# Kernel tuning notes

Measured on AMD Instinct MI355X. Metric: run time of the kernel, lower is better.

Reference implementation:

```python
import jax, jax.numpy as jnp
import numpy as np

Q = 16          # ELM-AE hidden size (init kwarg)
SPATIAL = 14    # spatial size of x[round(len(x)/2)] = x[2]
WH = SPATIAL * SPATIAL


def _zscore_nan(X):
    # torch_zscore(x, axis=0): normalize each pixel column over the z channels,
    # torch.std is unbiased (ddof=1); then torch.nan_to_num.
    mu = jnp.mean(X, axis=0)
    sd = jnp.std(X, axis=0, ddof=1)
    return jnp.nan_to_num((X - mu) / sd)


def _elm_member(xm, W):
    # xm: [b, z, wh] resized+flattened activation map; W: [Q, z] random encoder.
    def per_sample(Xs):                 # Xs: [z, wh]
        Xn = _zscore_nan(Xs)            # [z, wh]
        H = jax.nn.sigmoid(W @ Xn)      # [Q, wh] hidden representation
        B = Xn @ jnp.linalg.pinv(H)     # [z, Q]  closed-form AE decoder weights
        return jnp.var(B, axis=1, ddof=1)  # [z] variance pooling (Q > 1 branch)
    return jax.vmap(per_sample)(xm)     # [b, z]


def _forward(x0, x1, x2, x3, W0, W1, W2, W3):
    feats = []
    for xm, W in zip((x0, x1, x2, x3), (W0, W1, W2, W3)):
        b, c = xm.shape[0], xm.shape[1]
        xr = jax.image.resize(xm, (b, c, SPATIAL, SPATIAL), method='bilinear')
        feats.append(_elm_member(xr.reshape(b, c, WH), W))
    return jnp.concatenate(feats, axis=1)  # [b, sum_z] == torch.stack(out)


def setup_inputs() -> dict:
    key = jax.random.key(0)
    ks = jax.random.split(key, 8)
    shapes = [(32, 256, 56, 56), (32, 512, 28, 28), (32, 1024, 14, 14), (32, 2048, 7, 7)]
    inp = {}
    for i, s in enumerate(shapes):
        inp[f'x{i}'] = jax.random.normal(ks[i], s, dtype=jnp.float32)
        # original: zscored LCG pseudo-random weights, shape [Q, z]
        inp[f'W{i}'] = jax.random.normal(ks[4 + i], (Q, s[1]), dtype=jnp.float32)
    return inp


def reference(x0, x1, x2, x3, W0, W1, W2, W3):
    return _forward(x0, x1, x2, x3, W0, W1, W2, W3)
```

## Files before the change

kernel.cpp:

```cpp
#include <hip/hip_runtime.h>
#include <math.h>

#define NB 32
#define NQ 16
#define NP 196
#define OUTW 3840
#define HM_STRIDE (NQ * NP + NQ)
#define HM3_STRIDE (NQ * 49 + NQ)

template<int N>
__device__ __forceinline__ int calc_w(int i, float* w, int& lo) {
  constexpr float inv = (float)N / 14.0f;
  constexpr float ks  = (inv > 1.0f) ? inv : 1.0f;
  constexpr float rks = 1.0f / ks;
  float sf = ((float)i + 0.5f) * inv - 0.5f;
  int l = (int)ceilf(sf - ks);
  int h = (int)floorf(sf + ks);
  if (l < 0) l = 0;
  if (h > N - 1) h = N - 1;
  int n = h - l + 1;
  float sum = 0.f;
  for (int k = 0; k < n; ++k) {
    float t = 1.0f - fabsf((float)(l + k) - sf) * rks;
    t = t > 0.f ? t : 0.f;
    w[k] = t; sum += t;
  }
  float r = 1.0f / sum;
  for (int k = 0; k < n; ++k) w[k] *= r;
  for (int k = n; k < 8; ++k) w[k] = 0.f;
  lo = l;
  return n;
}

template<int N, int CH_BLK>
__global__ __launch_bounds__(256) void k_rs_mem(const float* __restrict__ x,
    const float* __restrict__ W, float* __restrict__ xr,
    float* __restrict__ part, int cm) {
  constexpr int TAPS = (N == 56) ? 8 : 4;
  constexpr int NROW = CH_BLK * N;
  constexpr int RV = N / 4;
  __shared__ float tmp[CH_BLK * N * 15];
  __shared__ float wxa[14 * 8], wya[14 * 8];
  __shared__ int lya[14], nya[14];
  __shared__ float wl[NQ * CH_BLK];
  const int t = threadIdx.x;
  const int s = blockIdx.x >> 5, chunk = blockIdx.x & 31;
  const int c0 = chunk * CH_BLK;

  if (t < 14)                 { int dum; calc_w<N>(t, &wxa[t * 8], dum); }
  else if (t >= 64 && t < 78) { int i = t - 64; nya[i] = calc_w<N>(i, &wya[i * 8], lya[i]); }
  for (int i = t; i < NQ * CH_BLK; i += 256) {
    int q = i / CH_BLK, cc = i - q * CH_BLK;
    wl[i] = W[q * cm + c0 + cc];
  }
  __syncthreads();

  for (int i = t; i < NROW; i += 256) {
    const int pl = i / N, r = i - pl * N;
    const float4* rp = (const float4*)(x + ((size_t)(s * cm + c0 + pl) * N + r) * N);
    float row[N];
#pragma unroll
    for (int j = 0; j < RV; ++j) {
      float4 f = rp[j];
      row[4 * j + 0] = f.x; row[4 * j + 1] = f.y;
      row[4 * j + 2] = f.z; row[4 * j + 3] = f.w;
    }
    float* td = &tmp[i * 15];
#pragma unroll
    for (int ox = 0; ox < 14; ++ox) {
      const int lx0 = (N == 56) ? (4 * ox - 2) : (2 * ox - 1);
      const int lx = lx0 < 0 ? 0 : lx0;
      float acc = 0.f;
#pragma unroll
      for (int k = 0; k < TAPS; ++k) {
        if (lx + k < N) acc = fmaf(wxa[ox * 8 + k], row[lx + k], acc);
      }
      td[ox] = acc;
    }
  }
  __syncthreads();

  if (t < NP) {
    const int oy = t / 14, ox = t - oy * 14;
    const int ny = nya[oy], ly = lya[oy];
    const float* wy = &wya[oy * 8];
    float s1 = 0.f, s2 = 0.f, y[NQ];
#pragma unroll
    for (int q = 0; q < NQ; ++q) y[q] = 0.f;
#pragma unroll
    for (int pl = 0; pl < CH_BLK; ++pl) {
      const float* tc = &tmp[(pl * N + ly) * 15 + ox];
      float acc = 0.f;
      for (int k = 0; k < ny; ++k) acc = fmaf(wy[k], tc[k * 15], acc);
      xr[((size_t)s * cm + c0 + pl) * NP + t] = acc;
      s1 += acc; s2 = fmaf(acc, acc, s2);
#pragma unroll
      for (int q = 0; q < NQ; ++q) y[q] = fmaf(wl[q * CH_BLK + pl], acc, y[q]);
    }
    float* pb = part + (size_t)(s * 32 + chunk) * 18 * NP + t;
    pb[0] = s1;
    pb[NP] = s2;
#pragma unroll
    for (int q = 0; q < NQ; ++q) pb[(size_t)(2 + q) * NP] = y[q];
  }
}

__global__ __launch_bounds__(256) void k_rs2(const float* __restrict__ x,
    const float* __restrict__ W, float* __restrict__ part) {
  const int t = threadIdx.x;
  if (t >= NP) return;
  const int s = blockIdx.x >> 5, chunk = blockIdx.x & 31;
  const int c0 = chunk * 32;
  const float* src = x + ((size_t)s * 1024 + c0) * NP + t;
  float s1 = 0.f, s2 = 0.f, y[NQ];
#pragma unroll
  for (int q = 0; q < NQ; ++q) y[q] = 0.f;
  for (int c = 0; c < 32; ++c) {
    float v = src[(size_t)c * NP];
    s1 += v; s2 = fmaf(v, v, s2);
#pragma unroll
    for (int q = 0; q < NQ; ++q) y[q] = fmaf(W[q * 1024 + c0 + c], v, y[q]);
  }
  float* pb = part + (size_t)(s * 32 + chunk) * 18 * NP + t;
  pb[0] = s1;
  pb[NP] = s2;
#pragma unroll
  for (int q = 0; q < NQ; ++q) pb[(size_t)(2 + q) * NP] = y[q];
}

__global__ __launch_bounds__(256) void k_rs3(const float* __restrict__ x,
    const float* __restrict__ W, float* __restrict__ part) {
  __shared__ __align__(16) float xl[64 * 49 + 16];
  __shared__ float wl[NQ * 64];
  __shared__ float w7a[14 * 8];
  __shared__ int l7a[14], n7a[14];
  const int t = threadIdx.x;
  const int s = blockIdx.x >> 5, chunk = blockIdx.x & 31;
  const int c0 = chunk * 64;

  if (t < 14) n7a[t] = calc_w<7>(t, &w7a[t * 8], l7a[t]);
  for (int i = t; i < NQ * 64; i += 256) {
    int q = i >> 6, cc = i & 63;
    wl[i] = W[q * 2048 + c0 + cc];
  }
  const float4* src4 = (const float4*)(x + ((size_t)s * 2048 + c0) * 49);
  float4* x4 = (float4*)xl;
  for (int i = t; i < 64 * 49 / 4; i += 256) x4[i] = src4[i];
  __syncthreads();

  if (t < NP) {
    const int oy = t / 14, ox = t - oy * 14;
    const int ly = l7a[oy], lx = l7a[ox];
    const float wy0 = w7a[oy * 8], wy1 = (n7a[oy] > 1) ? w7a[oy * 8 + 1] : 0.f;
    const float wx0 = w7a[ox * 8], wx1 = (n7a[ox] > 1) ? w7a[ox * 8 + 1] : 0.f;
    const int base0 = ly * 7 + lx;
    float s1 = 0.f, s2 = 0.f, y[NQ];
#pragma unroll
    for (int q = 0; q < NQ; ++q) y[q] = 0.f;
    for (int c = 0; c < 64; ++c) {
      const float* bb = &xl[c * 49 + base0];
      float v = wy0 * fmaf(wx1, bb[1], wx0 * bb[0]) + wy1 * fmaf(wx1, bb[8], wx0 * bb[7]);
      s1 += v; s2 = fmaf(v, v, s2);
#pragma unroll
      for (int q = 0; q < NQ; ++q) y[q] = fmaf(wl[q * 64 + c], v, y[q]);
    }
    float* pb = part + (size_t)(s * 32 + chunk) * 18 * NP + t;
    pb[0] = s1;
    pb[NP] = s2;
#pragma unroll
    for (int q = 0; q < NQ; ++q) pb[(size_t)(2 + q) * NP] = y[q];
  }
}

struct HeadArgs {
  const float* part[4];
  const float* W[4];
  float* hm[4];
  int cm[4];
};

__global__ __launch_bounds__(256) void k_head(HeadArgs A) {
  const int m = blockIdx.y, s = blockIdx.x, t = threadIdx.x;
  const int cm = A.cm[m];
  const float* W = A.W[m];
  const float* part = A.part[m];
  float* hm = A.hm[m];

  __shared__ float red[256];
  __shared__ float wsum[NQ];
  __shared__ float Hl[NQ * NP];
  __shared__ float HMl[NQ * NP];
  __shared__ float mul[NP], rsdl[NP];
  __shared__ float aug[16 * 33];
  __shared__ float Ml[256];
  __shared__ float el[NQ];
  __shared__ float w7[14 * 8];
  __shared__ int l7[14], n7[14];
  __shared__ float Radj[14 * 7];
  __shared__ float t2[NQ * 7 * 14];

  { int q = t >> 4, l = t & 15;
    float p = 0.f;
    for (int c = l; c < cm; c += 16) p += W[q * cm + c];
    red[t] = p; }
  __syncthreads();
  if (t < NQ) { float v = 0.f; for (int k = 0; k < 16; ++k) v += red[t * 16 + k]; wsum[t] = v; }
  __syncthreads();

  if (t < NP) {
    float s1 = 0.f, s2 = 0.f, y[NQ];
#pragma unroll
    for (int q = 0; q < NQ; ++q) y[q] = 0.f;
    for (int ch = 0; ch < 32; ++ch) {
      const float* pb = part + (size_t)(s * 32 + ch) * 18 * NP + t;
      s1 += pb[0];
      s2 += pb[NP];
#pragma unroll
      for (int q = 0; q < NQ; ++q) y[q] += pb[(size_t)(2 + q) * NP];
    }
    float mu = s1 / (float)cm;
    float var = (s2 - s1 * mu) / (float)(cm - 1);
    float rsd = (var > 0.f) ? (1.0f / sqrtf(var)) : 0.f;
    mul[t] = mu; rsdl[t] = rsd;
#pragma unroll
    for (int q = 0; q < NQ; ++q) {
      float arg = (y[q] - wsum[q] * mu) * rsd;
      Hl[q * NP + t] = 1.0f / (1.0f + expf(-arg));
    }
  }
  __syncthreads();

  { int q1 = t >> 4, q2 = t & 15;
    float g = 0.f;
    for (int p = 0; p < NP; ++p) g = fmaf(Hl[q1 * NP + p], Hl[q2 * NP + p], g);
    aug[q1 * 33 + q2] = g;
    aug[q1 * 33 + 16 + q2] = (q1 == q2) ? 1.0f : 0.f; }
  __syncthreads();

  for (int k = 0; k < 16; ++k) {
    float rpv = 1.0f / aug[k * 33 + k];
    __syncthreads();
    if (t < 32) aug[k * 33 + t] *= rpv;
    __syncthreads();
    int i = t >> 4, j = t & 15;
    float f = aug[i * 33 + k];
    __syncthreads();
    if (i != k) {
      aug[i * 33 + j]      -= f * aug[k * 33 + j];
      aug[i * 33 + 16 + j] -= f * aug[k * 33 + 16 + j];
    }
    __syncthreads();
  }
  { int i = t >> 4, j = t & 15; Ml[t] = aug[i * 33 + 16 + j]; }
  __syncthreads();

  if (t < NP) {
    float r_ = rsdl[t];
#pragma unroll
    for (int j = 0; j < NQ; ++j) {
      float acc = 0.f;
#pragma unroll
      for (int q = 0; q < NQ; ++q) acc = fmaf(Ml[j * 16 + q], Hl[q * NP + t], acc);
      HMl[j * NP + t] = acc * r_;
    }
  }
  __syncthreads();

  { int j = t >> 4, l = t & 15;
    float p = 0.f;
    for (int pp = l; pp < NP; pp += 16) p = fmaf(mul[pp], HMl[j * NP + pp], p);
    red[t] = p; }
  __syncthreads();
  if (t < NQ) { float v = 0.f; for (int k = 0; k < 16; ++k) v += red[t * 16 + k]; el[t] = v; }
  __syncthreads();

  if (m < 3) {
    float* dst = hm + (size_t)s * HM_STRIDE;
    for (int i = t; i < NQ * NP; i += 256) dst[i] = HMl[i];
    if (t < NQ) dst[NQ * NP + t] = el[t];
  } else {
    if (t < 14) n7[t] = calc_w<7>(t, &w7[t * 8], l7[t]);
    __syncthreads();
    if (t < 98) {
      int oy = t / 7, iy = t - oy * 7;
      int k = iy - l7[oy];
      Radj[oy * 7 + iy] = (k >= 0 && k < n7[oy]) ? w7[oy * 8 + k] : 0.f;
    }
    __syncthreads();
    for (int i = t; i < NQ * 7 * 14; i += 256) {
      int j = i / 98, rem = i - j * 98, iy = rem / 14, ox = rem - iy * 14;
      float acc = 0.f;
#pragma unroll
      for (int oy = 0; oy < 14; ++oy) acc = fmaf(Radj[oy * 7 + iy], HMl[j * NP + oy * 14 + ox], acc);
      t2[i] = acc;
    }
    __syncthreads();
    float* dst = hm + (size_t)s * HM3_STRIDE;
    for (int i = t; i < NQ * 49; i += 256) {
      int j = i / 49, rem = i - j * 49, iy = rem / 7, ix = rem - iy * 7;
      float acc = 0.f;
#pragma unroll
      for (int ox = 0; ox < 14; ++ox) acc = fmaf(Radj[ox * 7 + ix], t2[j * 98 + iy * 14 + ox], acc);
      dst[i] = acc;
    }
    if (t < NQ) dst[NQ * 49 + t] = el[t];
  }
}

#define CC3 32
struct VarArgs {
  const float* src[4];
  const float* hm[4];
  int cm[4];
  int ooff[4];
};

__global__ __launch_bounds__(512) void k_var(VarArgs A, float* __restrict__ out) {
  __shared__ __align__(16) float tile[CC3 * NP];
  __shared__ __align__(16) float hml[NQ * NP];
  __shared__ float el[NQ];
  int b = blockIdx.x;
  int m;
  if (b < 256)       { m = 0; }
  else if (b < 768)  { m = 1; b -= 256; }
  else if (b < 1792) { m = 2; b -= 768; }
  else               { m = 3; b -= 1792; }
  const int t = threadIdx.x;
  const int cc = t >> 4, j = t & 15;

  if (m < 3) {
    const int cm = A.cm[m];
    const int nch = cm / CC3;
    const int s = b / nch;
    const int ch = b % nch;
    const float4* src = (const float4*)(A.src[m] + ((size_t)s * cm + ch * CC3) * NP);
    float4* t4 = (float4*)tile;
    for (int i = t; i < CC3 * NP / 4; i += 512) t4[i] = src[i];
    const float4* hsrc = (const float4*)(A.hm[m] + (size_t)s * HM_STRIDE);
    float4* h4 = (float4*)hml;
    for (int i = t; i < NQ * NP / 4; i += 512) h4[i] = hsrc[i];
    if (t < NQ) el[t] = A.hm[m][(size_t)s * HM_STRIDE + NQ * NP + t];
    __syncthreads();

    const float4* tr = (const float4*)(tile + cc * NP);
    const float4* hr = (const float4*)(hml + j * NP);
    float acc = 0.f;
#pragma unroll 7
    for (int p4 = 0; p4 < NP / 4; ++p4) {
      float4 a = tr[p4], b2 = hr[p4];
      acc = fmaf(a.x, b2.x, acc);
      acc = fmaf(a.y, b2.y, acc);
      acc = fmaf(a.z, b2.z, acc);
      acc = fmaf(a.w, b2.w, acc);
    }
    float bv = acc - el[j];
    float s1 = bv;
    s1 += __shfl_xor(s1, 1, 16); s1 += __shfl_xor(s1, 2, 16);
    s1 += __shfl_xor(s1, 4, 16); s1 += __shfl_xor(s1, 8, 16);
    float mean = s1 * (1.0f / 16.0f);
    float d = bv - mean;
    float s2 = d * d;
    s2 += __shfl_xor(s2, 1, 16); s2 += __shfl_xor(s2, 2, 16);
    s2 += __shfl_xor(s2, 4, 16); s2 += __shfl_xor(s2, 8, 16);
    if (j == 0) out[(size_t)s * OUTW + A.ooff[m] + ch * CC3 + cc] = s2 * (1.0f / 15.0f);
  } else {
    const int s = b / 64;
    const int ch = b % 64;
    const float4* src = (const float4*)(A.src[3] + ((size_t)s * 2048 + ch * CC3) * 49);
    float4* t4 = (float4*)tile;
    for (int i = t; i < CC3 * 49 / 4; i += 512) t4[i] = src[i];
    const float4* hsrc = (const float4*)(A.hm[3] + (size_t)s * HM3_STRIDE);
    float4* h4 = (float4*)hml;
    for (int i = t; i < NQ * 49 / 4; i += 512) h4[i] = hsrc[i];
    if (t < NQ) el[t] = A.hm[3][(size_t)s * HM3_STRIDE + NQ * 49 + t];
    __syncthreads();

    const float* tr = tile + cc * 49;
    const float* hr = hml + j * 49;
    float acc = 0.f;
#pragma unroll
    for (int i = 0; i < 49; ++i) acc = fmaf(tr[i], hr[i], acc);
    float bv = acc - el[j];
    float s1 = bv;
    s1 += __shfl_xor(s1, 1, 16); s1 += __shfl_xor(s1, 2, 16);
    s1 += __shfl_xor(s1, 4, 16); s1 += __shfl_xor(s1, 8, 16);
    float mean = s1 * (1.0f / 16.0f);
    float d = bv - mean;
    float s2 = d * d;
    s2 += __shfl_xor(s2, 1, 16); s2 += __shfl_xor(s2, 2, 16);
    s2 += __shfl_xor(s2, 4, 16); s2 += __shfl_xor(s2, 8, 16);
    if (j == 0) out[(size_t)s * OUTW + 1792 + ch * CC3 + cc] = s2 * (1.0f / 15.0f);
  }
}

extern "C" void kernel_launch(void* const* d_in, const int* in_sizes, int n_in,
                              void* d_out, int out_size, void* d_ws, size_t ws_size,
                              hipStream_t stream) {
  const float* x0 = (const float*)d_in[0];
  const float* W0 = (const float*)d_in[1];
  const float* x1 = (const float*)d_in[2];
  const float* W1 = (const float*)d_in[3];
  const float* x2 = (const float*)d_in[4];
  const float* W2 = (const float*)d_in[5];
  const float* x3 = (const float*)d_in[6];
  const float* W3 = (const float*)d_in[7];
  float* out = (float*)d_out;
  float* ws = (float*)d_ws;

  float* xr0 = ws;
  float* xr1 = xr0 + (size_t)NB * 256 * NP;
  float* part0 = xr1 + (size_t)NB * 512 * NP;
  size_t plm = (size_t)NB * 32 * 18 * NP;
  float* part1 = part0 + plm;
  float* part2 = part1 + plm;
  float* part3 = part2 + plm;
  float* hm0 = part3 + plm;
  float* hm1 = hm0 + (size_t)NB * HM_STRIDE;
  float* hm2 = hm1 + (size_t)NB * HM_STRIDE;
  float* hm3 = hm2 + (size_t)NB * HM_STRIDE;

  k_rs_mem<56, 8><<<1024, 256, 0, stream>>>(x0, W0, xr0, part0, 256);
  k_rs_mem<28, 16><<<1024, 256, 0, stream>>>(x1, W1, xr1, part1, 512);
  k_rs2<<<1024, 256, 0, stream>>>(x2, W2, part2);
  k_rs3<<<1024, 256, 0, stream>>>(x3, W3, part3);

  HeadArgs A;
  A.part[0] = part0; A.part[1] = part1; A.part[2] = part2; A.part[3] = part3;
  A.W[0] = W0; A.W[1] = W1; A.W[2] = W2; A.W[3] = W3;
  A.hm[0] = hm0; A.hm[1] = hm1; A.hm[2] = hm2; A.hm[3] = hm3;
  A.cm[0] = 256; A.cm[1] = 512; A.cm[2] = 1024; A.cm[3] = 2048;
  k_head<<<dim3(NB, 4), 256, 0, stream>>>(A);

  VarArgs V;
  V.src[0] = xr0; V.src[1] = xr1; V.src[2] = x2; V.src[3] = x3;
  V.hm[0] = hm0; V.hm[1] = hm1; V.hm[2] = hm2; V.hm[3] = hm3;
  V.cm[0] = 256; V.cm[1] = 512; V.cm[2] = 1024; V.cm[3] = 2048;
  V.ooff[0] = 0; V.ooff[1] = 256; V.ooff[2] = 768; V.ooff[3] = 1792;
  k_var<<<3840, 512, 0, stream>>>(V, out);
  (void)in_sizes; (void)n_in; (void)out_size; (void)ws_size;
}
```

Measured before the change: 192.2 us.

## Coalesce horizontal resize loads with per-lane float4 and wavefront shuffles

Result: slower. 229.6 us (+19.4%).

```diff
diff --git a/kernel.cpp b/kernel.cpp
--- a/kernel.cpp
+++ b/kernel.cpp
@@ -32,50 +32,128 @@
   return n;
 }
 
-template<int N, int CH_BLK>
-__global__ __launch_bounds__(256) void k_rs_mem(const float* __restrict__ x,
+__global__ __launch_bounds__(256) void k_rs0(const float* __restrict__ x,
     const float* __restrict__ W, float* __restrict__ xr,
-    float* __restrict__ part, int cm) {
-  constexpr int TAPS = (N == 56) ? 8 : 4;
-  constexpr int NROW = CH_BLK * N;
-  constexpr int RV = N / 4;
+    float* __restrict__ part) {
+  constexpr int N = 56, CH_BLK = 8, cm = 256;
   __shared__ float tmp[CH_BLK * N * 15];
-  __shared__ float wxa[14 * 8], wya[14 * 8];
+  __shared__ float wxs[14 * 8];
+  __shared__ float wya[14 * 8];
   __shared__ int lya[14], nya[14];
   __shared__ float wl[NQ * CH_BLK];
   const int t = threadIdx.x;
   const int s = blockIdx.x >> 5, chunk = blockIdx.x & 31;
   const int c0 = chunk * CH_BLK;
 
-  if (t < 14)                 { int dum; calc_w<N>(t, &wxa[t * 8], dum); }
-  else if (t >= 64 && t < 78) { int i = t - 64; nya[i] = calc_w<N>(i, &wya[i * 8], lya[i]); }
+  if (t < 14) {
+    float w[8]; int lo; int n = calc_w<N>(t, w, lo);
+    int off = lo - (4 * t - 2);
+    for (int k = 0; k < 8; ++k) wxs[t * 8 + k] = 0.f;
+    for (int k = 0; k < n; ++k) wxs[t * 8 + off + k] = w[k];
+  } else if (t >= 64 && t < 78) {
+    int i = t - 64; nya[i] = calc_w<N>(i, &wya[i * 8], lya[i]);
+  }
   for (int i = t; i < NQ * CH_BLK; i += 256) {
     int q = i / CH_BLK, cc = i - q * CH_BLK;
     wl[i] = W[q * cm + c0 + cc];
   }
   __syncthreads();
 
-  for (int i = t; i < NROW; i += 256) {
-    const int pl = i / N, r = i - pl * N;
-    const float4* rp = (const float4*)(x + ((size_t)(s * cm + c0 + pl) * N + r) * N);
-    float row[N];
-#pragma unroll
-    for (int j = 0; j < RV; ++j) {
-      float4 f = rp[j];
-      row[4 * j + 0] = f.x; row[4 * j + 1] = f.y;
-      row[4 * j + 2] = f.z; row[4 * j + 3] = f.w;
-    }
-    float* td = &tmp[i * 15];
-#pragma unroll
-    for (int ox = 0; ox < 14; ++ox) {
-      const int lx0 = (N == 56) ? (4 * ox - 2) : (2 * ox - 1);
-      const int lx = lx0 < 0 ? 0 : lx0;
+  {
+    const int wv = t >> 6, lane = t & 63;
+    const int rr = lane / 14, j = lane - rr * 14;
+    const bool act = lane < 56;
+#pragma unroll 4
+    for (int g = wv; g < 112; g += 4) {
+      const int R = g * 4 + rr;
+      const int pl = R / N, r = R - pl * N;
+      float4 v = make_float4(0.f, 0.f, 0.f, 0.f);
+      if (act) v = *(const float4*)(x + (((size_t)(s * cm + c0 + pl)) * N + r) * N + 4 * j);
+      float vmz = __shfl(v.z, lane - 1);
+      float vmw = __shfl(v.w, lane - 1);
+      float vpx = __shfl(v.x, lane + 1);
+      float vpy = __shfl(v.y, lane + 1);
+      const float* wx = &wxs[j * 8];
+      float acc = wx[0] * vmz + wx[1] * vmw + wx[2] * v.x + wx[3] * v.y
+                + wx[4] * v.z + wx[5] * v.w + wx[6] * vpx + wx[7] * vpy;
+      if (act) tmp[R * 15 + j] = acc;
+    }
+  }
+  __syncthreads();
+
+  if (t < NP) {
+    const int oy = t / 14, ox = t - oy * 14;
+    const int ny = nya[oy], ly = lya[oy];
+    const float* wy = &wya[oy * 8];
+    float s1 = 0.f, s2 = 0.f, y[NQ];
+#pragma unroll
+    for (int q = 0; q < NQ; ++q) y[q] = 0.f;
+#pragma unroll
+    for (int pl = 0; pl < CH_BLK; ++pl) {
+      const float* tc = &tmp[(pl * N + ly) * 15 + ox];
       float acc = 0.f;
-#pragma unroll
-      for (int k = 0; k < TAPS; ++k) {
-        if (lx + k < N) acc = fmaf(wxa[ox * 8 + k], row[lx + k], acc);
+      for (int k = 0; k < ny; ++k) acc = fmaf(wy[k], tc[k * 15], acc);
+      xr[((size_t)s * cm + c0 + pl) * NP + t] = acc;
+      s1 += acc; s2 = fmaf(acc, acc, s2);
+#pragma unroll
+      for (int q = 0; q < NQ; ++q) y[q] = fmaf(wl[q * CH_BLK + pl], acc, y[q]);
+    }
+    float* pb = part + (size_t)(s * 32 + chunk) * 18 * NP + t;
+    pb[0] = s1;
+    pb[NP] = s2;
+#pragma unroll
+    for (int q = 0; q < NQ; ++q) pb[(size_t)(2 + q) * NP] = y[q];
+  }
+}
+
+__global__ __launch_bounds__(256) void k_rs1(const float* __restrict__ x,
+    const float* __restrict__ W, float* __restrict__ xr,
+    float* __restrict__ part) {
+  constexpr int N = 28, CH_BLK = 16, cm = 512;
+  __shared__ float tmp[CH_BLK * N * 15];
+  __shared__ float wxs[14 * 4];
+  __shared__ float wya[14 * 8];
+  __shared__ int lya[14], nya[14];
+  __shared__ float wl[NQ * CH_BLK];
+  const int t = threadIdx.x;
+  const int s = blockIdx.x >> 5, chunk = blockIdx.x & 31;
+  const int c0 = chunk * CH_BLK;
+
+  if (t < 14) {
+    float w[8]; int lo; int n = calc_w<N>(t, w, lo);
+    int off = lo - (2 * t - 1);
+    for (int k = 0; k < 4; ++k) wxs[t * 4 + k] = 0.f;
+    for (int k = 0; k < n; ++k) wxs[t * 4 + off + k] = w[k];
+  } else if (t >= 64 && t < 78) {
+    int i = t - 64; nya[i] = calc_w<N>(i, &wya[i * 8], lya[i]);
+  }
+  for (int i = t; i < NQ * CH_BLK; i += 256) {
+    int q = i / CH_BLK, cc = i - q * CH_BLK;
+    wl[i] = W[q * cm + c0 + cc];
+  }
+  __syncthreads();
+
+  {
+    const int wv = t >> 6, lane = t & 63;
+    const int rr = lane / 7, j = lane - rr * 7;
+    const bool act = lane < 56;
+#pragma unroll 4
+    for (int g = wv; g < 56; g += 4) {
+      const int R = g * 8 + rr;
+      const int pl = R / N, r = R - pl * N;
+      float4 v = make_float4(0.f, 0.f, 0.f, 0.f);
+      if (act) v = *(const float4*)(x + (((size_t)(s * cm + c0 + pl)) * N + r) * N + 4 * j);
+      float vmw = __shfl(v.w, lane - 1);
+      float vpx = __shfl(v.x, lane + 1);
+      const int ox0 = 2 * j;
+      const float* w0 = &wxs[ox0 * 4];
+      const float* w1 = &wxs[(ox0 + 1) * 4];
+      float acc0 = w0[0] * vmw + w0[1] * v.x + w0[2] * v.y + w0[3] * v.z;
+      float acc1 = w1[0] * v.y + w1[1] * v.z + w1[2] * v.w + w1[3] * vpx;
+      if (act) {
+        tmp[R * 15 + ox0] = acc0;
+        tmp[R * 15 + ox0 + 1] = acc1;
       }
-      td[ox] = acc;
     }
   }
   __syncthreads();
@@ -419,8 +497,8 @@
   float* hm2 = hm1 + (size_t)NB * HM_STRIDE;
   float* hm3 = hm2 + (size_t)NB * HM_STRIDE;
 
-  k_rs_mem<56, 8><<<1024, 256, 0, stream>>>(x0, W0, xr0, part0, 256);
-  k_rs_mem<28, 16><<<1024, 256, 0, stream>>>(x1, W1, xr1, part1, 512);
+  k_rs0<<<1024, 256, 0, stream>>>(x0, W0, xr0, part0);
+  k_rs1<<<1024, 256, 0, stream>>>(x1, W1, xr1, part1);
   k_rs2<<<1024, 256, 0, stream>>>(x2, W2, part2);
   k_rs3<<<1024, 256, 0, stream>>>(x3, W3, part3);
 
```
